# Kernel tuning notes

Measured on AMD Instinct MI355X. Metric: run time of the kernel, lower is better.

The kernel has to match this reference:

```python
import math
import jax, jax.numpy as jnp
import numpy as np

B, S, E, H = 4, 2048, 1024, 16
D = E // H


def setup_inputs() -> dict:
    key = jax.random.key(0)
    k1, k2, k3 = jax.random.split(key, 3)
    return {
        "hidden_state": jax.random.normal(k1, (B, S, E), dtype=jnp.float32),
        "attention_mask": jnp.zeros((B, 1, 1, S), dtype=jnp.float32),
        "W_attn": jax.random.normal(k2, (E, 3 * E), dtype=jnp.float32) * 0.02,
        "b_attn": jnp.zeros((3 * E,), dtype=jnp.float32),
        "W_proj": jax.random.normal(k3, (E, E), dtype=jnp.float32) * 0.02,
        "b_proj": jnp.zeros((E,), dtype=jnp.float32),
    }


def reference(hidden_state, attention_mask, W_attn, b_attn, W_proj, b_proj):
    b, s, e = hidden_state.shape
    d = e // H
    # c_attn (HF Conv1D): x @ W + b -> [B,S,3E]
    x = hidden_state @ W_attn + b_attn
    q, k, v = jnp.split(x, 3, axis=-1)
    # split heads -> [B,H,S,D]
    q = q.reshape(b, s, H, d).transpose(0, 2, 1, 3)
    k = k.reshape(b, s, H, d).transpose(0, 2, 1, 3)
    v = v.reshape(b, s, H, d).transpose(0, 2, 1, 3)
    # scores [B,H,S,S]; scale=True divides by sqrt(d_head)
    w = jnp.einsum("bhqd,bhkd->bhqk", q, k) / math.sqrt(d)
    causal = jnp.tril(jnp.ones((s, s), dtype=w.dtype))[None, None]
    w = w * causal + (-10000.0) * (1.0 - causal)
    w = w + attention_mask
    w = jax.nn.softmax(w, axis=-1)  # attn_dropout p=0 (eval)
    out = jnp.einsum("bhqk,bhkd->bhqd", w, v)
    # merge heads -> [B,S,E]
    out = out.transpose(0, 2, 1, 3).reshape(b, s, e)
    # c_proj; resid_dropout p=0 (eval)
    return out @ W_proj + b_proj
```

## Files before the change

kernel.cpp:

```cpp
#include <hip/hip_runtime.h>
#include <hip/hip_bf16.h>

typedef __attribute__((ext_vector_type(4))) float f32x4;
typedef __attribute__((ext_vector_type(8))) short bf16x8;

#define B_SZ  4
#define S_LEN 2048
#define EMB   1024
#define NH    16
#define DH    64
#define E3    3072
#define QKLD  2048
#define LOG2E 1.4426950408889634f
#define SC2   (0.125f * LOG2E)
#define MSTAT 14.0f

__device__ __forceinline__ void gload_lds16(const void* g, void* l) {
  __builtin_amdgcn_global_load_lds((const __attribute__((address_space(1))) void*)g,
                                   (__attribute__((address_space(3))) void*)l, 16, 0, 0);
}

__device__ __forceinline__ float bf2f(unsigned short u) {
  union { unsigned int i; float f; } c;
  c.i = (unsigned int)u << 16;
  return c.f;
}

__global__ void cvt_bf16_kernel(const float* __restrict__ in,
                                __hip_bfloat16* __restrict__ out, int n) {
  const int i = (blockIdx.x * 256 + threadIdx.x) * 4;
  if (i >= n) return;
  const float4 v = *(const float4*)(in + i);
  __align__(8) __hip_bfloat16 o[4];
  o[0] = __float2bfloat16(v.x); o[1] = __float2bfloat16(v.y);
  o[2] = __float2bfloat16(v.z); o[3] = __float2bfloat16(v.w);
  *(uint2*)(out + i) = *(const uint2*)o;
}

__global__ __launch_bounds__(256)
void transpose_cvt(const float* __restrict__ in, __hip_bfloat16* __restrict__ out,
                   int R, int C) {
  __shared__ float tile[32][33];
  const int tx = threadIdx.x & 31, ty = threadIdx.x >> 5;
  const int c = blockIdx.x * 32 + tx;
#pragma unroll
  for (int i = 0; i < 32; i += 8)
    tile[ty + i][tx] = in[(size_t)(blockIdx.y * 32 + ty + i) * C + c];
  __syncthreads();
  const int r2 = blockIdx.y * 32 + tx;
#pragma unroll
  for (int i = 0; i < 32; i += 8)
    out[(size_t)(blockIdx.x * 32 + ty + i) * R + r2] = __float2bfloat16(tile[tx][ty + i]);
}

__global__ __launch_bounds__(256)
void gemm_bt_f32(const __hip_bfloat16* __restrict__ A, const __hip_bfloat16* __restrict__ BT,
                 const float* __restrict__ bias, float* __restrict__ Cout,
                 int M, int N, int K, int ldc) {
  __shared__ __align__(16) __hip_bfloat16 As[128 * 32];
  __shared__ __align__(16) __hip_bfloat16 Bs[128 * 32];
  const int tid = threadIdx.x;
  const int lane = tid & 63, w = tid >> 6;
  const int lr = lane & 15, lg = lane >> 4;
  const int wr = w >> 1, wc = w & 1;
  const int m0 = blockIdx.x * 128, n0 = blockIdx.y * 128;

  f32x4 acc[4][4] = {};

  for (int k0 = 0; k0 < K; k0 += 32) {
    __syncthreads();
#pragma unroll
    for (int rr = 0; rr < 2; ++rr) {
      const int base = rr * 4096 + w * 1024;
      const int idx = base + lane * 16;
      const int row = idx >> 6;
      const int col = (idx & 63) >> 1;
      gload_lds16(A + (size_t)(m0 + row) * K + k0 + col, (char*)As + base);
      gload_lds16(BT + (size_t)(n0 + row) * K + k0 + col, (char*)Bs + base);
    }
    __syncthreads();
    bf16x8 af[4], bg[4];
#pragma unroll
    for (int m = 0; m < 4; ++m)
      af[m] = *(const bf16x8*)&As[(wr * 64 + m * 16 + lr) * 32 + lg * 8];
#pragma unroll
    for (int n = 0; n < 4; ++n)
      bg[n] = *(const bf16x8*)&Bs[(wc * 64 + n * 16 + lr) * 32 + lg * 8];
#pragma unroll
    for (int m = 0; m < 4; ++m)
#pragma unroll
      for (int n = 0; n < 4; ++n)
        acc[m][n] = __builtin_amdgcn_mfma_f32_16x16x32_bf16(af[m], bg[n], acc[m][n], 0, 0, 0);
  }

#pragma unroll
  for (int m = 0; m < 4; ++m)
#pragma unroll
    for (int n = 0; n < 4; ++n) {
      const int col = n0 + wc * 64 + n * 16 + lr;
      const float bv = bias[col];
#pragma unroll
      for (int r = 0; r < 4; ++r) {
        const int rowg = m0 + wr * 64 + m * 16 + lg * 4 + r;
        Cout[(size_t)rowg * ldc + col] = acc[m][n][r] + bv;
      }
    }
}

#define SBAR() { __builtin_amdgcn_s_barrier(); __builtin_amdgcn_sched_barrier(0); }
#define VMCNT(N) asm volatile("s_waitcnt vmcnt(" #N ")" ::: "memory")

#define STG_A(T, H, BUF) { \
    const __hip_bfloat16* s_ = pA + (size_t)((H) * 128) * 1024 + (T) * 64; \
    gload_lds16(s_, (BUF) + (H) * 16384 + w * 1024 + lane * 16); \
    gload_lds16(s_ + 65536, (BUF) + (H) * 16384 + 8192 + w * 1024 + lane * 16); }

#define STG_B(T, H, BUF) { \
    const __hip_bfloat16* s_ = pB + (size_t)((H) * 128) * 1024 + (T) * 64; \
    gload_lds16(s_, (BUF) + (H) * 16384 + w * 1024 + lane * 16); \
    gload_lds16(s_ + 65536, (BUF) + (H) * 16384 + 8192 + w * 1024 + lane * 16); }

#define RD_A(BUF, MH) { _Pragma("unroll") for (int m_ = 0; m_ < 4; ++m_) { \
    a[m_][0] = *(const bf16x8*)((BUF) + arow + ((MH) * 64 + m_ * 16) * 128 + sw0); \
    a[m_][1] = *(const bf16x8*)((BUF) + arow + ((MH) * 64 + m_ * 16) * 128 + sw1); } }

#define RD_B(BUF, NH, BARR) { _Pragma("unroll") for (int n_ = 0; n_ < 2; ++n_) { \
    BARR[n_][0] = *(const bf16x8*)((BUF) + brow + ((NH) * 32 + n_ * 16) * 128 + sw0); \
    BARR[n_][1] = *(const bf16x8*)((BUF) + brow + ((NH) * 32 + n_ * 16) * 128 + sw1); } }

#define MQUAD(MH, NH, BARR) { __builtin_amdgcn_s_setprio(1); \
    _Pragma("unroll") for (int m_ = 0; m_ < 4; ++m_) \
    _Pragma("unroll") for (int n_ = 0; n_ < 2; ++n_) \
    _Pragma("unroll") for (int k_ = 0; k_ < 2; ++k_) \
      acc[(MH)*4+m_][(NH)*2+n_] = __builtin_amdgcn_mfma_f32_16x16x32_bf16( \
          a[m_][k_], BARR[n_][k_], acc[(MH)*4+m_][(NH)*2+n_], 0, 0, 0); \
    __builtin_amdgcn_s_setprio(0); }

__global__ __launch_bounds__(512, 2)
void gemm_qkv_8ph(const __hip_bfloat16* __restrict__ A, const __hip_bfloat16* __restrict__ BT,
                  const float* __restrict__ bias, __hip_bfloat16* __restrict__ qkOut,
                  __hip_bfloat16* __restrict__ vt) {
  __shared__ __attribute__((aligned(16))) char lds[131072];
  char* const As0 = lds;
  char* const As1 = lds + 32768;
  char* const Bs0 = lds + 65536;
  char* const Bs1 = lds + 98304;

  const int tid = threadIdx.x;
  const int lane = tid & 63, w = tid >> 6;
  const int lr = lane & 15, lg = lane >> 4, lg4 = lg * 4;
  const int wm = w >> 2, wn = w & 3;
  const int m0 = blockIdx.x * 256, n0 = blockIdx.y * 256;

  const int srl = lane >> 3;
  const int scol = ((lane & 7) ^ srl) * 8;
  const __hip_bfloat16* pA = A + (size_t)(m0 + w * 8 + srl) * 1024 + scol;
  const __hip_bfloat16* pB = BT + (size_t)(n0 + w * 8 + srl) * 1024 + scol;

  const int sw0 = (lg ^ (lr & 7)) << 4;
  const int sw1 = sw0 ^ 0x40;
  const int arow = (wm * 128 + lr) * 128;
  const int brow = (wn * 64 + lr) * 128;

  f32x4 acc[8][4] = {};
  bf16x8 a[4][2], b0[2][2], b1[2][2];

  STG_A(0, 0, As0); STG_B(0, 0, Bs0); STG_A(0, 1, As0); STG_B(0, 1, Bs0); STG_A(1, 0, As1);
  VMCNT(2);
  SBAR();

  auto iter = [&](int t0, bool more) {
    RD_A(As0, 0); RD_B(Bs0, 0, b0);
    STG_B(t0 + 1, 0, Bs1);
    SBAR(); MQUAD(0, 0, b0); SBAR();
    RD_B(Bs0, 1, b1);
    STG_A(t0 + 1, 1, As1);
    SBAR(); MQUAD(0, 1, b1); SBAR();
    RD_A(As0, 1); RD_B(Bs0, 0, b0);
    STG_B(t0 + 1, 1, Bs1);
    SBAR(); MQUAD(1, 0, b0); SBAR();
    RD_B(Bs0, 1, b1);
    if (more) { STG_A(t0 + 2, 0, As0); VMCNT(2); } else { VMCNT(0); }
    SBAR(); MQUAD(1, 1, b1); SBAR();
    RD_A(As1, 0); RD_B(Bs1, 0, b0);
    if (more) STG_B(t0 + 2, 0, Bs0);
    SBAR(); MQUAD(0, 0, b0); SBAR();
    RD_B(Bs1, 1, b1);
    if (more) STG_A(t0 + 2, 1, As0);
    SBAR(); MQUAD(0, 1, b1); SBAR();
    RD_A(As1, 1); RD_B(Bs1, 0, b0);
    if (more) STG_B(t0 + 2, 1, Bs0);
    SBAR(); MQUAD(1, 0, b0); SBAR();
    RD_B(Bs1, 1, b1);
    if (more) { STG_A(t0 + 3, 0, As1); VMCNT(2); }
    SBAR(); MQUAD(1, 1, b1); SBAR();
  };

#pragma unroll 1
  for (int i = 0; i < 7; ++i) iter(2 * i, true);
  iter(14, false);

  if (n0 >= 2 * EMB) {
#pragma unroll
    for (int m8 = 0; m8 < 8; ++m8) {
      const int rowg0 = m0 + wm * 128 + m8 * 16 + lg4;
      const int bz = rowg0 >> 11, sloc = rowg0 & (S_LEN - 1);
#pragma unroll
      for (int n4 = 0; n4 < 4; ++n4) {
        const int col = n0 + wn * 64 + n4 * 16 + lr;
        const int c2 = col - 2 * EMB;
        const int hh = c2 >> 6, dd = c2 & 63;
        const float bv = bias[col];
        __align__(8) __hip_bfloat16 pb[4];
#pragma unroll
        for (int r = 0; r < 4; ++r) pb[r] = __float2bfloat16(acc[m8][n4][r] + bv);
        *(uint2*)&vt[(size_t)((bz * NH + hh) * DH + dd) * S_LEN + sloc] = *(const uint2*)pb;
      }
    }
  } else {
#pragma unroll
    for (int m8 = 0; m8 < 8; ++m8) {
#pragma unroll
      for (int n4 = 0; n4 < 4; ++n4) {
        const int col = n0 + wn * 64 + n4 * 16 + lr;
        const float bv = bias[col];
#pragma unroll
        for (int r = 0; r < 4; ++r) {
          const int rowg = m0 + wm * 128 + m8 * 16 + lg4 + r;
          qkOut[(size_t)rowg * QKLD + col] = __float2bfloat16(acc[m8][n4][r] + bv);
        }
      }
    }
  }
}


template <bool DIAG>
__device__ __forceinline__ void qstep(const char* Ks, const char* Vs,
                                      __hip_bfloat16 (*Psw)[72], const __hip_bfloat16* Msb,
                                      int msoff, const bf16x8 (&aq)[2], f32x4 (&acc)[4],
                                      float& lrun, int lr, int lg, int lg4, int wq) {
  f32x4 sacc[4] = {};
  __builtin_amdgcn_s_setprio(1);
#pragma unroll
  for (int kt = 0; kt < 4; ++kt)
#pragma unroll
    for (int ks = 0; ks < 2; ++ks) {
      const bf16x8 kb = *(const bf16x8*)(Ks + (kt * 16 + lr) * 128 +
                                         (((ks * 4 + lg) ^ (lr & 7)) << 4));
      sacc[kt] = __builtin_amdgcn_mfma_f32_16x16x32_bf16(kb, aq[ks], sacc[kt], 0, 0, 0);
    }
  __builtin_amdgcn_s_setprio(0);
#pragma unroll
  for (int kt = 0; kt < 4; ++kt) {
    const ushort4 mb = *(const ushort4*)&Msb[msoff + kt * 16 + lg4];
    float pp[4];
    __align__(8) __hip_bfloat16 pb[4];
#pragma unroll
    for (int r = 0; r < 4; ++r) {
      float sv = sacc[kt][r] * SC2 + bf2f(((const unsigned short*)&mb)[r]);
      if (DIAG && (kt * 16 + lg4 + r > wq)) sv = -1.0e9f;
      pp[r] = exp2f(sv);
      pb[r] = __float2bfloat16(pp[r]);
    }
    lrun += (pp[0] + pp[1]) + (pp[2] + pp[3]);
    *(uint2*)&Psw[lr][kt * 16 + lg4] = *(const uint2*)pb;
  }
#pragma unroll
  for (int ks = 0; ks < 2; ++ks) {
    const bf16x8 pa = *(const bf16x8*)&Psw[lr][ks * 32 + lg * 8];
    __builtin_amdgcn_s_setprio(1);
#pragma unroll
    for (int dt = 0; dt < 4; ++dt) {
      const bf16x8 vb = *(const bf16x8*)(Vs + (dt * 16 + lr) * 128 +
                                         (((ks * 4 + lg) ^ (lr & 7)) << 4));
      acc[dt] = __builtin_amdgcn_mfma_f32_16x16x32_bf16(pa, vb, acc[dt], 0, 0, 0);
    }
    __builtin_amdgcn_s_setprio(0);
  }
}

template <bool DIAGA>
__device__ __forceinline__ void qstep2(const char* Ks, const char* Vs,
                                       __hip_bfloat16 (*PsA)[72], __hip_bfloat16 (*PsB)[72],
                                       const __hip_bfloat16* Msb, int msoff,
                                       const bf16x8 (&aqA)[2], const bf16x8 (&aqB)[2],
                                       f32x4 (&accA)[4], f32x4 (&accB)[4],
                                       float& lA, float& lB, int lr, int lg, int lg4, int wq) {
  f32x4 sA[4] = {}, sB[4] = {};
  __builtin_amdgcn_s_setprio(1);
#pragma unroll
  for (int kt = 0; kt < 4; ++kt)
#pragma unroll
    for (int ks = 0; ks < 2; ++ks) {
      const bf16x8 kb = *(const bf16x8*)(Ks + (kt * 16 + lr) * 128 +
                                         (((ks * 4 + lg) ^ (lr & 7)) << 4));
      sA[kt] = __builtin_amdgcn_mfma_f32_16x16x32_bf16(kb, aqA[ks], sA[kt], 0, 0, 0);
      sB[kt] = __builtin_amdgcn_mfma_f32_16x16x32_bf16(kb, aqB[ks], sB[kt], 0, 0, 0);
    }
  __builtin_amdgcn_s_setprio(0);
#pragma unroll
  for (int kt = 0; kt < 4; ++kt) {
    const ushort4 mb = *(const ushort4*)&Msb[msoff + kt * 16 + lg4];
    float pA[4], pB[4];
    __align__(8) __hip_bfloat16 bA[4], bB[4];
#pragma unroll
    for (int r = 0; r < 4; ++r) {
      const float mkr = bf2f(((const unsigned short*)&mb)[r]);
      float svA = sA[kt][r] * SC2 + mkr;
      if (DIAGA && (kt * 16 + lg4 + r > wq)) svA = -1.0e9f;
      const float svB = sB[kt][r] * SC2 + mkr;
      pA[r] = exp2f(svA); bA[r] = __float2bfloat16(pA[r]);
      pB[r] = exp2f(svB); bB[r] = __float2bfloat16(pB[r]);
    }
    lA += (pA[0] + pA[1]) + (pA[2] + pA[3]);
    lB += (pB[0] + pB[1]) + (pB[2] + pB[3]);
    *(uint2*)&PsA[lr][kt * 16 + lg4] = *(const uint2*)bA;
    *(uint2*)&PsB[lr][kt * 16 + lg4] = *(const uint2*)bB;
  }
#pragma unroll
  for (int ks = 0; ks < 2; ++ks) {
    const bf16x8 paA = *(const bf16x8*)&PsA[lr][ks * 32 + lg * 8];
    const bf16x8 paB = *(const bf16x8*)&PsB[lr][ks * 32 + lg * 8];
    __builtin_amdgcn_s_setprio(1);
#pragma unroll
    for (int dt = 0; dt < 4; ++dt) {
      const bf16x8 vb = *(const bf16x8*)(Vs + (dt * 16 + lr) * 128 +
                                         (((ks * 4 + lg) ^ (lr & 7)) << 4));
      accA[dt] = __builtin_amdgcn_mfma_f32_16x16x32_bf16(paA, vb, accA[dt], 0, 0, 0);
      accB[dt] = __builtin_amdgcn_mfma_f32_16x16x32_bf16(paB, vb, accB[dt], 0, 0, 0);
    }
    __builtin_amdgcn_s_setprio(0);
  }
}

#define STAGE_LOAD_BUMP()                                                          \
  {                                                                                \
    kpre[0] = *(const bf16x8*)kcur;                                                \
    kpre[1] = *(const bf16x8*)(kcur + 8 * QKLD);                                   \
    vpre[0] = *(const bf16x8*)vcur;                                                \
    vpre[1] = *(const bf16x8*)(vcur + 8 * S_LEN);                                  \
    kcur += 64 * QKLD;                                                             \
    vcur += 64;                                                                    \
  }

#define TILE_SYNC(PREFETCH)                                                        \
  {                                                                                \
    __syncthreads();                                                               \
    *(bf16x8*)kw0 = kpre[0];                                                       \
    *(bf16x8*)(kw0 + 1024) = kpre[1];                                              \
    *(bf16x8*)vw0 = vpre[0];                                                       \
    *(bf16x8*)(vw0 + 1024) = vpre[1];                                              \
    __syncthreads();                                                               \
    if (PREFETCH) STAGE_LOAD_BUMP();                                               \
  }

__global__ __launch_bounds__(256, 4)
void flash_attn7(const __hip_bfloat16* __restrict__ qk, const __hip_bfloat16* __restrict__ vt,
                 const float* __restrict__ amask, __hip_bfloat16* __restrict__ aout) {
  const int j = blockIdx.x;
  const int g = (j & 7) + 8 * (j >> 7);
  const int x = (j >> 3) & 15;
  const int h = g >> 2, bz = g & 3;

  const int tid = threadIdx.x;
  const int lane = tid & 63, w = tid >> 6;
  const int lr = lane & 15, lg = lane >> 4, lg4 = lg * 4;
  const int wq = w * 16 + lr;

  const int qta = x, qtb = 31 - x;

  __shared__ __align__(16) __hip_bfloat16 Ks[64 * 64];
  __shared__ __align__(16) __hip_bfloat16 Vs[64 * 64];
  __shared__ __align__(16) __hip_bfloat16 Ps[4][2][16][72];
  __shared__ __align__(8)  __hip_bfloat16 Msb[S_LEN];

  {
    const int e = tid * 8;
    const f32x4 m0v = *(const f32x4*)&amask[bz * S_LEN + e];
    const f32x4 m1v = *(const f32x4*)&amask[bz * S_LEN + e + 4];
    __align__(16) __hip_bfloat16 mb[8];
#pragma unroll
    for (int jj = 0; jj < 4; ++jj) {
      mb[jj]     = __float2bfloat16(m0v[jj] * LOG2E - MSTAT);
      mb[jj + 4] = __float2bfloat16(m1v[jj] * LOG2E - MSTAT);
    }
    *(uint4*)&Msb[e] = *(const uint4*)mb;
  }

  bf16x8 aqA[2], aqB[2];
  {
    const __hip_bfloat16* qpA =
        qk + (size_t)(bz * S_LEN + qta * 64 + w * 16 + lr) * QKLD + h * DH + lg * 8;
    aqA[0] = *(const bf16x8*)qpA; aqA[1] = *(const bf16x8*)(qpA + 32);
    const __hip_bfloat16* qpB =
        qk + (size_t)(bz * S_LEN + qtb * 64 + w * 16 + lr) * QKLD + h * DH + lg * 8;
    aqB[0] = *(const bf16x8*)qpB; aqB[1] = *(const bf16x8*)(qpB + 32);
  }

  f32x4 accA[4] = {}, accB[4] = {};
  float lA = 0.f, lB = 0.f;

  const __hip_bfloat16* kcur = qk + (size_t)bz * S_LEN * QKLD + EMB + h * DH +
                               (size_t)(w * 16 + (lane >> 3)) * QKLD + (lane & 7) * 8;
  const __hip_bfloat16* vcur = vt + (size_t)((bz * NH + h) * DH + w * 16 + (lane >> 3)) * S_LEN +
                               (lane & 7) * 8;
  char* kw0 = (char*)Ks + (w * 16 + (lane >> 3)) * 128 + (((lane & 7) ^ (lane >> 3)) << 4);
  char* vw0 = (char*)Vs + (w * 16 + (lane >> 3)) * 128 + (((lane & 7) ^ (lane >> 3)) << 4);

  bf16x8 kpre[2], vpre[2];
  STAGE_LOAD_BUMP();

  int msoff = 0;
  for (int t = 0; t < qta; ++t) {
    TILE_SYNC(true);
    qstep2<false>((char*)Ks, (char*)Vs, Ps[w][0], Ps[w][1], Msb, msoff,
                  aqA, aqB, accA, accB, lA, lB, lr, lg, lg4, wq);
    msoff += 64;
  }
  TILE_SYNC(true);
  qstep2<true>((char*)Ks, (char*)Vs, Ps[w][0], Ps[w][1], Msb, msoff,
               aqA, aqB, accA, accB, lA, lB, lr, lg, lg4, wq);
  msoff += 64;
  for (int t = qta + 1; t < qtb; ++t) {
    TILE_SYNC(true);
    qstep<false>((char*)Ks, (char*)Vs, Ps[w][1], Msb, msoff, aqB, accB, lB, lr, lg, lg4, wq);
    msoff += 64;
  }
  TILE_SYNC(false);
  qstep<true>((char*)Ks, (char*)Vs, Ps[w][1], Msb, msoff, aqB, accB, lB, lr, lg, lg4, wq);

  lA += __shfl_xor(lA, 16); lA += __shfl_xor(lA, 32);
  lB += __shfl_xor(lB, 16); lB += __shfl_xor(lB, 32);
  float lqA[4], lqB[4];
#pragma unroll
  for (int r = 0; r < 4; ++r) {
    lqA[r] = __shfl(lA, lg4 + r);
    lqB[r] = __shfl(lB, lg4 + r);
  }
#pragma unroll
  for (int dt = 0; dt < 4; ++dt)
#pragma unroll
    for (int r = 0; r < 4; ++r) {
      const int qA = qta * 64 + w * 16 + lg4 + r;
      aout[(size_t)(bz * S_LEN + qA) * EMB + h * DH + dt * 16 + lr] =
          __float2bfloat16(accA[dt][r] / lqA[r]);
      const int qB = qtb * 64 + w * 16 + lg4 + r;
      aout[(size_t)(bz * S_LEN + qB) * EMB + h * DH + dt * 16 + lr] =
          __float2bfloat16(accB[dt][r] / lqB[r]);
    }
}

extern "C" void kernel_launch(void* const* d_in, const int* in_sizes, int n_in,
                              void* d_out, int out_size, void* d_ws, size_t ws_size,
                              hipStream_t stream) {
  const float* hidden = (const float*)d_in[0];
  const float* amask  = (const float*)d_in[1];
  const float* W_attn = (const float*)d_in[2];
  const float* b_attn = (const float*)d_in[3];
  const float* W_proj = (const float*)d_in[4];
  const float* b_proj = (const float*)d_in[5];
  float* out = (float*)d_out;

  char* ws = (char*)d_ws;
  __hip_bfloat16* hbf   = (__hip_bfloat16*)(ws);
  __hip_bfloat16* WaT   = (__hip_bfloat16*)(ws + 16777216);
  __hip_bfloat16* WpT   = (__hip_bfloat16*)(ws + 23068672);
  __hip_bfloat16* qkQK  = (__hip_bfloat16*)(ws + 25165824);
  __hip_bfloat16* vt    = (__hip_bfloat16*)(ws + 58720256);
  __hip_bfloat16* aoutb = (__hip_bfloat16*)(ws + 75497472);

  cvt_bf16_kernel<<<dim3(8192), dim3(256), 0, stream>>>(hidden, hbf, B_SZ * S_LEN * EMB);
  transpose_cvt<<<dim3(96, 32), dim3(256), 0, stream>>>(W_attn, WaT, EMB, E3);
  transpose_cvt<<<dim3(32, 32), dim3(256), 0, stream>>>(W_proj, WpT, EMB, EMB);
  gemm_qkv_8ph<<<dim3(32, 12), dim3(512), 0, stream>>>(hbf, WaT, b_attn, qkQK, vt);
  flash_attn7<<<dim3(1024), dim3(256), 0, stream>>>(qkQK, vt, amask, aoutb);
  gemm_bt_f32<<<dim3(64, 8), dim3(256), 0, stream>>>(aoutb, WpT, b_proj, out,
                                                     8192, EMB, EMB, EMB);
}
```

Baseline: 188.8 us.

## Reuse pipelined 256x256 GEMM for output projection and reorder attention tile mapping

The simple 128x128 output-projection GEMM is replaced by the 8-phase pipelined 256x256 GEMM that already handles QKV, templated to gain an fp32 bias epilogue. This targets the weaker LDS staging and lack of overlap in the old projection kernel. Only 128 blocks are launched for this GEMM, which may underfill the GPU. The attention block-to-query-tile mapping is also rotated per group, meant to spread causal workload more evenly across concurrently scheduled blocks.

```diff
diff --git a/kernel.cpp b/kernel.cpp
--- a/kernel.cpp
+++ b/kernel.cpp
@@ -53,60 +53,6 @@
     out[(size_t)(blockIdx.x * 32 + ty + i) * R + r2] = __float2bfloat16(tile[tx][ty + i]);
 }
 
-__global__ __launch_bounds__(256)
-void gemm_bt_f32(const __hip_bfloat16* __restrict__ A, const __hip_bfloat16* __restrict__ BT,
-                 const float* __restrict__ bias, float* __restrict__ Cout,
-                 int M, int N, int K, int ldc) {
-  __shared__ __align__(16) __hip_bfloat16 As[128 * 32];
-  __shared__ __align__(16) __hip_bfloat16 Bs[128 * 32];
-  const int tid = threadIdx.x;
-  const int lane = tid & 63, w = tid >> 6;
-  const int lr = lane & 15, lg = lane >> 4;
-  const int wr = w >> 1, wc = w & 1;
-  const int m0 = blockIdx.x * 128, n0 = blockIdx.y * 128;
-
-  f32x4 acc[4][4] = {};
-
-  for (int k0 = 0; k0 < K; k0 += 32) {
-    __syncthreads();
-#pragma unroll
-    for (int rr = 0; rr < 2; ++rr) {
-      const int base = rr * 4096 + w * 1024;
-      const int idx = base + lane * 16;
-      const int row = idx >> 6;
-      const int col = (idx & 63) >> 1;
-      gload_lds16(A + (size_t)(m0 + row) * K + k0 + col, (char*)As + base);
-      gload_lds16(BT + (size_t)(n0 + row) * K + k0 + col, (char*)Bs + base);
-    }
-    __syncthreads();
-    bf16x8 af[4], bg[4];
-#pragma unroll
-    for (int m = 0; m < 4; ++m)
-      af[m] = *(const bf16x8*)&As[(wr * 64 + m * 16 + lr) * 32 + lg * 8];
-#pragma unroll
-    for (int n = 0; n < 4; ++n)
-      bg[n] = *(const bf16x8*)&Bs[(wc * 64 + n * 16 + lr) * 32 + lg * 8];
-#pragma unroll
-    for (int m = 0; m < 4; ++m)
-#pragma unroll
-      for (int n = 0; n < 4; ++n)
-        acc[m][n] = __builtin_amdgcn_mfma_f32_16x16x32_bf16(af[m], bg[n], acc[m][n], 0, 0, 0);
-  }
-
-#pragma unroll
-  for (int m = 0; m < 4; ++m)
-#pragma unroll
-    for (int n = 0; n < 4; ++n) {
-      const int col = n0 + wc * 64 + n * 16 + lr;
-      const float bv = bias[col];
-#pragma unroll
-      for (int r = 0; r < 4; ++r) {
-        const int rowg = m0 + wr * 64 + m * 16 + lg * 4 + r;
-        Cout[(size_t)rowg * ldc + col] = acc[m][n][r] + bv;
-      }
-    }
-}
-
 #define SBAR() { __builtin_amdgcn_s_barrier(); __builtin_amdgcn_sched_barrier(0); }
 #define VMCNT(N) asm volatile("s_waitcnt vmcnt(" #N ")" ::: "memory")
 
@@ -136,10 +82,11 @@
           a[m_][k_], BARR[n_][k_], acc[(MH)*4+m_][(NH)*2+n_], 0, 0, 0); \
     __builtin_amdgcn_s_setprio(0); }
 
+template <int EPI>
 __global__ __launch_bounds__(512, 2)
-void gemm_qkv_8ph(const __hip_bfloat16* __restrict__ A, const __hip_bfloat16* __restrict__ BT,
-                  const float* __restrict__ bias, __hip_bfloat16* __restrict__ qkOut,
-                  __hip_bfloat16* __restrict__ vt) {
+void gemm_8ph(const __hip_bfloat16* __restrict__ A, const __hip_bfloat16* __restrict__ BT,
+              const float* __restrict__ bias, void* __restrict__ Cout,
+              __hip_bfloat16* __restrict__ vt) {
   __shared__ __attribute__((aligned(16))) char lds[131072];
   char* const As0 = lds;
   char* const As1 = lds + 32768;
@@ -200,7 +147,7 @@
   for (int i = 0; i < 7; ++i) iter(2 * i, true);
   iter(14, false);
 
-  if (n0 >= 2 * EMB) {
+  if (EPI == 0 && n0 >= 2 * EMB) {
 #pragma unroll
     for (int m8 = 0; m8 < 8; ++m8) {
       const int rowg0 = m0 + wm * 128 + m8 * 16 + lg4;
@@ -217,7 +164,7 @@
         *(uint2*)&vt[(size_t)((bz * NH + hh) * DH + dd) * S_LEN + sloc] = *(const uint2*)pb;
       }
     }
-  } else {
+  } else if (EPI == 0) {
 #pragma unroll
     for (int m8 = 0; m8 < 8; ++m8) {
 #pragma unroll
@@ -227,7 +174,21 @@
 #pragma unroll
         for (int r = 0; r < 4; ++r) {
           const int rowg = m0 + wm * 128 + m8 * 16 + lg4 + r;
-          qkOut[(size_t)rowg * QKLD + col] = __float2bfloat16(acc[m8][n4][r] + bv);
+          ((__hip_bfloat16*)Cout)[(size_t)rowg * QKLD + col] = __float2bfloat16(acc[m8][n4][r] + bv);
+        }
+      }
+    }
+  } else {
+#pragma unroll
+    for (int m8 = 0; m8 < 8; ++m8) {
+#pragma unroll
+      for (int n4 = 0; n4 < 4; ++n4) {
+        const int col = n0 + wn * 64 + n4 * 16 + lr;
+        const float bv = bias[col];
+#pragma unroll
+        for (int r = 0; r < 4; ++r) {
+          const int rowg = m0 + wm * 128 + m8 * 16 + lg4 + r;
+          ((float*)Cout)[(size_t)rowg * EMB + col] = acc[m8][n4][r] + bv;
         }
       }
     }
@@ -356,11 +317,11 @@
   }
 
 __global__ __launch_bounds__(256, 4)
-void flash_attn7(const __hip_bfloat16* __restrict__ qk, const __hip_bfloat16* __restrict__ vt,
+void flash_attn8(const __hip_bfloat16* __restrict__ qk, const __hip_bfloat16* __restrict__ vt,
                  const float* __restrict__ amask, __hip_bfloat16* __restrict__ aout) {
   const int j = blockIdx.x;
   const int g = (j & 7) + 8 * (j >> 7);
-  const int x = (j >> 3) & 15;
+  const int x = (((j >> 3) & 15) + (((j >> 8) & 3) << 2)) & 15;
   const int h = g >> 2, bz = g & 3;
 
   const int tid = threadIdx.x;
@@ -473,8 +434,7 @@
   cvt_bf16_kernel<<<dim3(8192), dim3(256), 0, stream>>>(hidden, hbf, B_SZ * S_LEN * EMB);
   transpose_cvt<<<dim3(96, 32), dim3(256), 0, stream>>>(W_attn, WaT, EMB, E3);
   transpose_cvt<<<dim3(32, 32), dim3(256), 0, stream>>>(W_proj, WpT, EMB, EMB);
-  gemm_qkv_8ph<<<dim3(32, 12), dim3(512), 0, stream>>>(hbf, WaT, b_attn, qkQK, vt);
-  flash_attn7<<<dim3(1024), dim3(256), 0, stream>>>(qkQK, vt, amask, aoutb);
-  gemm_bt_f32<<<dim3(64, 8), dim3(256), 0, stream>>>(aoutb, WpT, b_proj, out,
-                                                     8192, EMB, EMB, EMB);
-}
+  gemm_8ph<0><<<dim3(32, 12), dim3(512), 0, stream>>>(hbf, WaT, b_attn, qkQK, vt);
+  flash_attn8<<<dim3(1024), dim3(256), 0, stream>>>(qkQK, vt, amask, aoutb);
+  gemm_8ph<1><<<dim3(32, 4), dim3(512), 0, stream>>>(aoutb, WpT, b_proj, out, nullptr);
+}
```

After: 187.9 us. About the same (-0.5%).

## Restage QKV GEMM prefetch in paired A/B loads and rotate attention tile order

Applied to the files above, without the earlier changes.

The QKV GEMM's staging is reorganized. A and B half-tiles for the next k-step are now issued together early in each phase, the B register fragments are reused across the two M halves instead of being re-read from LDS, and the wait before buffer swap becomes a full vmcnt(0). The flash-attention kernel also rotates the query-tile index by block group, spreading long and short causal work differently across CUs. The GEMM change trades prefetch depth (full drain instead of partial waits) for fewer LDS reads, which can expose global-load latency.

```diff
diff --git a/kernel.cpp b/kernel.cpp
--- a/kernel.cpp
+++ b/kernel.cpp
@@ -110,15 +110,13 @@
 #define SBAR() { __builtin_amdgcn_s_barrier(); __builtin_amdgcn_sched_barrier(0); }
 #define VMCNT(N) asm volatile("s_waitcnt vmcnt(" #N ")" ::: "memory")
 
-#define STG_A(T, H, BUF) { \
-    const __hip_bfloat16* s_ = pA + (size_t)((H) * 128) * 1024 + (T) * 64; \
-    gload_lds16(s_, (BUF) + (H) * 16384 + w * 1024 + lane * 16); \
-    gload_lds16(s_ + 65536, (BUF) + (H) * 16384 + 8192 + w * 1024 + lane * 16); }
-
-#define STG_B(T, H, BUF) { \
-    const __hip_bfloat16* s_ = pB + (size_t)((H) * 128) * 1024 + (T) * 64; \
-    gload_lds16(s_, (BUF) + (H) * 16384 + w * 1024 + lane * 16); \
-    gload_lds16(s_ + 65536, (BUF) + (H) * 16384 + 8192 + w * 1024 + lane * 16); }
+#define STG2(T, H, BA, BB) { \
+    const __hip_bfloat16* sa_ = pA + (size_t)((H) * 128) * 1024 + (T) * 64; \
+    gload_lds16(sa_, (BA) + (H) * 16384 + w * 1024 + lane * 16); \
+    gload_lds16(sa_ + 65536, (BA) + (H) * 16384 + 8192 + w * 1024 + lane * 16); \
+    const __hip_bfloat16* sb_ = pB + (size_t)((H) * 128) * 1024 + (T) * 64; \
+    gload_lds16(sb_, (BB) + (H) * 16384 + w * 1024 + lane * 16); \
+    gload_lds16(sb_ + 65536, (BB) + (H) * 16384 + 8192 + w * 1024 + lane * 16); }
 
 #define RD_A(BUF, MH) { _Pragma("unroll") for (int m_ = 0; m_ < 4; ++m_) { \
     a[m_][0] = *(const bf16x8*)((BUF) + arow + ((MH) * 64 + m_ * 16) * 128 + sw0); \
@@ -165,34 +163,30 @@
   f32x4 acc[8][4] = {};
   bf16x8 a[4][2], b0[2][2], b1[2][2];
 
-  STG_A(0, 0, As0); STG_B(0, 0, Bs0); STG_A(0, 1, As0); STG_B(0, 1, Bs0); STG_A(1, 0, As1);
-  VMCNT(2);
+  STG2(0, 0, As0, Bs0); STG2(0, 1, As0, Bs0);
+  VMCNT(0);
   SBAR();
 
   auto iter = [&](int t0, bool more) {
     RD_A(As0, 0); RD_B(Bs0, 0, b0);
-    STG_B(t0 + 1, 0, Bs1);
+    STG2(t0 + 1, 0, As1, Bs1);
     SBAR(); MQUAD(0, 0, b0); SBAR();
     RD_B(Bs0, 1, b1);
-    STG_A(t0 + 1, 1, As1);
+    STG2(t0 + 1, 1, As1, Bs1);
     SBAR(); MQUAD(0, 1, b1); SBAR();
-    RD_A(As0, 1); RD_B(Bs0, 0, b0);
-    STG_B(t0 + 1, 1, Bs1);
+    RD_A(As0, 1);
     SBAR(); MQUAD(1, 0, b0); SBAR();
-    RD_B(Bs0, 1, b1);
-    if (more) { STG_A(t0 + 2, 0, As0); VMCNT(2); } else { VMCNT(0); }
+    VMCNT(0);
     SBAR(); MQUAD(1, 1, b1); SBAR();
     RD_A(As1, 0); RD_B(Bs1, 0, b0);
-    if (more) STG_B(t0 + 2, 0, Bs0);
+    if (more) STG2(t0 + 2, 0, As0, Bs0);
     SBAR(); MQUAD(0, 0, b0); SBAR();
     RD_B(Bs1, 1, b1);
-    if (more) STG_A(t0 + 2, 1, As0);
+    if (more) STG2(t0 + 2, 1, As0, Bs0);
     SBAR(); MQUAD(0, 1, b1); SBAR();
-    RD_A(As1, 1); RD_B(Bs1, 0, b0);
-    if (more) STG_B(t0 + 2, 1, Bs0);
+    RD_A(As1, 1);
     SBAR(); MQUAD(1, 0, b0); SBAR();
-    RD_B(Bs1, 1, b1);
-    if (more) { STG_A(t0 + 3, 0, As1); VMCNT(2); }
+    if (more) VMCNT(0);
     SBAR(); MQUAD(1, 1, b1); SBAR();
   };
 
@@ -233,7 +227,6 @@
     }
   }
 }
-
 
 template <bool DIAG>
 __device__ __forceinline__ void qstep(const char* Ks, const char* Vs,
@@ -356,11 +349,11 @@
   }
 
 __global__ __launch_bounds__(256, 4)
-void flash_attn7(const __hip_bfloat16* __restrict__ qk, const __hip_bfloat16* __restrict__ vt,
+void flash_attn8(const __hip_bfloat16* __restrict__ qk, const __hip_bfloat16* __restrict__ vt,
                  const float* __restrict__ amask, __hip_bfloat16* __restrict__ aout) {
   const int j = blockIdx.x;
   const int g = (j & 7) + 8 * (j >> 7);
-  const int x = (j >> 3) & 15;
+  const int x = (((j >> 3) & 15) + (((j >> 8) & 3) << 2)) & 15;
   const int h = g >> 2, bz = g & 3;
 
   const int tid = threadIdx.x;
@@ -474,7 +467,7 @@
   transpose_cvt<<<dim3(96, 32), dim3(256), 0, stream>>>(W_attn, WaT, EMB, E3);
   transpose_cvt<<<dim3(32, 32), dim3(256), 0, stream>>>(W_proj, WpT, EMB, EMB);
   gemm_qkv_8ph<<<dim3(32, 12), dim3(512), 0, stream>>>(hbf, WaT, b_attn, qkQK, vt);
-  flash_attn7<<<dim3(1024), dim3(256), 0, stream>>>(qkQK, vt, amask, aoutb);
+  flash_attn8<<<dim3(1024), dim3(256), 0, stream>>>(qkQK, vt, amask, aoutb);
   gemm_bt_f32<<<dim3(64, 8), dim3(256), 0, stream>>>(aoutb, WpT, b_proj, out,
                                                      8192, EMB, EMB, EMB);
 }
```

Result: no change. 186.4 us (-1.3%).
